# Performance work log

Measured on AMD Instinct MI355X. Metric: run time of the kernel, lower is better.

Reference implementation:

```python
import jax, jax.numpy as jnp
import numpy as np

# Dimensions
B, S, F, PATCH, D, H, NL, DFF, HOR = 512, 336, 12, 6, 512, 8, 6, 2048, 24
NP = S // PATCH        # 56 temporal patches
DH = D // H            # head dim = 64
EPS = 1e-5


def layer_norm(x, g, b):
    m = jnp.mean(x, axis=-1, keepdims=True)
    v = jnp.mean(jnp.square(x - m), axis=-1, keepdims=True)
    return (x - m) * jax.lax.rsqrt(v + EPS) * g + b


def alibi_bias(n_heads, n):
    # slopes = 2^(-8h/H), h = 1..H (standard ALiBi, H power of 2)
    slopes = 2.0 ** (-8.0 * jnp.arange(1, n_heads + 1, dtype=jnp.float32) / n_heads)
    pos = jnp.arange(n, dtype=jnp.float32)
    dist = jnp.abs(pos[:, None] - pos[None, :])         # [n, n]
    return -slopes[:, None, None] * dist                # [H, n, n]


def setup_inputs() -> dict:
    key = jax.random.key(0)
    ks = jax.random.split(key, 16)
    g = lambda k, shape: jax.random.normal(k, shape, dtype=jnp.float32) * 0.02
    return {
        "x": jax.random.normal(ks[0], (B, S, F), dtype=jnp.float32),
        "patch_W": g(ks[1], (PATCH * F, D)),
        "patch_b": jnp.zeros((D,), jnp.float32),
        "pos": g(ks[2], (NP, D)),
        "ln1_g": jnp.ones((NL, D), jnp.float32),
        "ln1_b": jnp.zeros((NL, D), jnp.float32),
        "Wq": g(ks[3], (NL, D, D)), "bq": jnp.zeros((NL, D), jnp.float32),
        "Wk": g(ks[4], (NL, D, D)), "bk": jnp.zeros((NL, D), jnp.float32),
        "Wv": g(ks[5], (NL, D, D)), "bv": jnp.zeros((NL, D), jnp.float32),
        "Wo": g(ks[6], (NL, D, D)), "bo": jnp.zeros((NL, D), jnp.float32),
        "ln2_g": jnp.ones((NL, D), jnp.float32),
        "ln2_b": jnp.zeros((NL, D), jnp.float32),
        "W1": g(ks[7], (NL, D, DFF)), "b1": jnp.zeros((NL, DFF), jnp.float32),
        "W2": g(ks[8], (NL, DFF, D)), "b2": jnp.zeros((NL, D), jnp.float32),
        "fn_g": jnp.ones((D,), jnp.float32),
        "fn_b": jnp.zeros((D,), jnp.float32),
        "head_W": g(ks[9], (D, HOR)),
        "head_b": jnp.zeros((HOR,), jnp.float32),
    }


def reference(x, patch_W, patch_b, pos, ln1_g, ln1_b, Wq, bq, Wk, bk, Wv, bv,
              Wo, bo, ln2_g, ln2_b, W1, b1, W2, b2, fn_g, fn_b, head_W, head_b):
    # Temporal patch embedding: (B,S,F) -> (B,NP,PATCH*F) -> Linear -> +pos
    h = x.reshape(B, NP, PATCH * F) @ patch_W + patch_b + pos  # [B, NP, D]
    bias = alibi_bias(H, NP)                                   # [H, NP, NP]
    scale = 1.0 / np.sqrt(DH).astype(np.float32)
    for l in range(NL):
        # Pre-LN multi-head attention with ALiBi temporal decay bias
        hn = layer_norm(h, ln1_g[l], ln1_b[l])
        q = (hn @ Wq[l] + bq[l]).reshape(B, NP, H, DH)
        k = (hn @ Wk[l] + bk[l]).reshape(B, NP, H, DH)
        v = (hn @ Wv[l] + bv[l]).reshape(B, NP, H, DH)
        sc = jnp.einsum('bqhd,bkhd->bhqk', q, k) * scale + bias[None]
        a = jax.nn.softmax(sc, axis=-1)
        o = jnp.einsum('bhqk,bkhd->bqhd', a, v).reshape(B, NP, D)
        h = h + (o @ Wo[l] + bo[l])
        # Pre-LN feedforward
        hn2 = layer_norm(h, ln2_g[l], ln2_b[l])
        h = h + (jax.nn.gelu(hn2 @ W1[l] + b1[l]) @ W2[l] + b2[l])
    pooled = jnp.mean(h, axis=1)                               # [B, D]
    out = layer_norm(pooled, fn_g, fn_b) @ head_W + head_b     # [B, HOR]
    return out
```

## Files before the change

### kernel.cpp

```cpp
#include <hip/hip_runtime.h>
#include <hip/hip_bf16.h>
#include <math.h>

#define D_      512
#define NPATCH  56
#define DFF_    2048
#define NLAYER  6
#define HEADS   8
#define DH_     64
#define HOR_    24
#define BATCH_  512
#define NTOK_   (BATCH_ * NPATCH)
#define KPAD    96

typedef __hip_bfloat16 bf16;
typedef __bf16 bf16x8 __attribute__((ext_vector_type(8)));
typedef float  f32x4  __attribute__((ext_vector_type(4)));

__device__ __forceinline__ void gload_lds16(const void* g, void* lds) {
    __builtin_amdgcn_global_load_lds(
        (const __attribute__((address_space(1))) unsigned int*)g,
        (__attribute__((address_space(3))) unsigned int*)lds, 16, 0, 0);
}

__device__ __forceinline__ float block_sum256(float v) {
    __shared__ float sm[4];
    const int lane = threadIdx.x & 63;
    const int w    = threadIdx.x >> 6;
    #pragma unroll
    for (int o = 32; o > 0; o >>= 1) v += __shfl_down(v, o);
    __syncthreads();
    if (lane == 0) sm[w] = v;
    __syncthreads();
    return sm[0] + sm[1] + sm[2] + sm[3];
}

__device__ __forceinline__ float gelu_fast(float xg) {
    const float e = __expf(1.5957691216057308f * (xg + 0.044715f * xg * xg * xg));
    return xg - xg * __builtin_amdgcn_rcpf(1.f + e);
}

__global__ __launch_bounds__(256) void transpose_bf16_k(
    const float* __restrict__ in, bf16* __restrict__ out, int R, int C,
    size_t in_ls, size_t out_ls)
{
    __shared__ float t[32][33];
    in  += (size_t)blockIdx.z * in_ls;
    out += (size_t)blockIdx.z * out_ls;
    const int c0 = blockIdx.x * 32, r0 = blockIdx.y * 32;
    const int x = threadIdx.x & 31, y = threadIdx.x >> 5;
    #pragma unroll
    for (int i = 0; i < 4; i++)
        t[y + i * 8][x] = in[(size_t)(r0 + y + i * 8) * C + c0 + x];
    __syncthreads();
    #pragma unroll
    for (int i = 0; i < 4; i++)
        out[(size_t)(c0 + y + i * 8) * R + r0 + x] = __float2bfloat16(t[x][y + i * 8]);
}

__global__ __launch_bounds__(256) void pwt_k(
    const float* __restrict__ W, bf16* __restrict__ out)
{
    const int idx = blockIdx.x * 256 + threadIdx.x;
    if (idx >= D_ * KPAD) return;
    const int n = idx / KPAD, kk = idx % KPAD;
    out[idx] = (kk < 72) ? __float2bfloat16(W[kk * D_ + n]) : __float2bfloat16(0.f);
}

__global__ __launch_bounds__(256) void xpad_k(
    const float* __restrict__ x, bf16* __restrict__ out)
{
    const size_t idx = (size_t)blockIdx.x * 256 + threadIdx.x;
    if (idx >= (size_t)NTOK_ * KPAD) return;
    const size_t row = idx / KPAD;
    const int kk = (int)(idx - row * KPAD);
    out[idx] = (kk < 72) ? __float2bfloat16(x[row * 72 + kk]) : __float2bfloat16(0.f);
}

__global__ __launch_bounds__(256) void bqkv_k(
    const float* __restrict__ bq, const float* __restrict__ bk,
    const float* __restrict__ bv, float* __restrict__ o)
{
    const int idx = blockIdx.x * 256 + threadIdx.x;
    if (idx >= NLAYER * 3 * D_) return;
    const int l = idx / (3 * D_), n = idx % (3 * D_);
    float v;
    if      (n < D_)     v = bq[l * D_ + n];
    else if (n < 2 * D_) v = bk[l * D_ + n - D_];
    else                 v = bv[l * D_ + n - 2 * D_];
    o[idx] = v;
}

__global__ __launch_bounds__(256) void layernorm_bf16_k(
    const bf16* __restrict__ x, const float* __restrict__ g,
    const float* __restrict__ b, bf16* __restrict__ y)
{
    const int w = threadIdx.x >> 6, lane = threadIdx.x & 63;
    const size_t row = (size_t)blockIdx.x * 4 + w;
    const bf16x8 a8 = *(const bf16x8*)((const __bf16*)x + row * D_ + lane * 8);
    float a[8];
    #pragma unroll
    for (int i = 0; i < 8; i++) a[i] = (float)a8[i];
    float s = 0.f;
    #pragma unroll
    for (int i = 0; i < 8; i++) s += a[i];
    #pragma unroll
    for (int o = 32; o > 0; o >>= 1) s += __shfl_xor(s, o);
    const float mean = s * (1.f / 512.f);
    float d[8];
    #pragma unroll
    for (int i = 0; i < 8; i++) d[i] = a[i] - mean;
    float v = 0.f;
    #pragma unroll
    for (int i = 0; i < 8; i++) v += d[i] * d[i];
    #pragma unroll
    for (int o = 32; o > 0; o >>= 1) v += __shfl_xor(v, o);
    const float rstd = rsqrtf(v * (1.f / 512.f) + 1e-5f);
    const float4 g0 = *(const float4*)(g + lane * 8);
    const float4 g1 = *(const float4*)(g + lane * 8 + 4);
    const float4 b0 = *(const float4*)(b + lane * 8);
    const float4 b1 = *(const float4*)(b + lane * 8 + 4);
    const float gg[8] = {g0.x, g0.y, g0.z, g0.w, g1.x, g1.y, g1.z, g1.w};
    const float bb[8] = {b0.x, b0.y, b0.z, b0.w, b1.x, b1.y, b1.z, b1.w};
    bf16x8 o8;
    #pragma unroll
    for (int i = 0; i < 8; i++) o8[i] = (__bf16)(d[i] * rstd * gg[i] + bb[i]);
    *(bf16x8*)((__bf16*)y + row * D_ + lane * 8) = o8;
}

template<bool GELU, bool RESID, bool POS, bool QKVSPLIT>
__global__ __launch_bounds__(512, 4) void gemm_bf16_k(
    const bf16* __restrict__ A, const bf16* __restrict__ Bt,
    const float* __restrict__ bias, const bf16* __restrict__ resid,
    const float* __restrict__ pos, bf16* __restrict__ Cp,
    bf16* __restrict__ vt, int M, int N, int K, int nx)
{
    __shared__ __align__(16) bf16 ABs[3][384 * 32];
    const int tid  = threadIdx.x;
    const int wid  = tid >> 6;
    const int lane = tid & 63;

    const int nwg = gridDim.x;
    const int q8 = nwg >> 3, r8 = nwg & 7;
    const int xcd = blockIdx.x & 7, idx8 = blockIdx.x >> 3;
    const int swz = (xcd < r8 ? xcd * (q8 + 1) : r8 * (q8 + 1) + (xcd - r8) * q8) + idx8;
    const int n0 = (swz % nx) * 256;
    const int m0 = (swz / nx) * 128;
    const int wr = wid >> 2, wc = wid & 3;

    f32x4 acc[4][4];
    #pragma unroll
    for (int m = 0; m < 4; m++)
        #pragma unroll
        for (int n = 0; n < 4; n++) acc[m][n] = f32x4{0.f, 0.f, 0.f, 0.f};

    const int srow = lane >> 2;
    const int schunk = ((lane & 3) ^ ((lane >> 3) & 3)) * 8;
    const bf16* sp[3];
    int soff[3];
    #pragma unroll
    for (int i = 0; i < 3; i++) {
        const int s = wid * 3 + i;
        soff[i] = s * 512;
        sp[i] = (s < 8)
            ? A  + (size_t)(m0 + s * 16 + srow) * K + schunk
            : Bt + (size_t)(n0 + (s - 8) * 16 + srow) * K + schunk;
    }

    const int fr = lane & 15;
    const int qg = lane >> 4;
    const int roff = fr * 32 + ((qg ^ ((fr >> 1) & 3)) * 8);

    const int nt = K >> 5;
    #define STAGE(buf, kt)  do {                                   \
        gload_lds16(sp[0] + ((kt) << 5), &ABs[buf][soff[0]]);      \
        gload_lds16(sp[1] + ((kt) << 5), &ABs[buf][soff[1]]);      \
        gload_lds16(sp[2] + ((kt) << 5), &ABs[buf][soff[2]]); } while (0)

    STAGE(0, 0);
    STAGE(1, 1);

    int cur = 0, nxt = 2;
    for (int t = 0; t < nt; t++) {
        if (t < nt - 1) asm volatile("s_waitcnt vmcnt(3)" ::: "memory");
        else            asm volatile("s_waitcnt vmcnt(0)" ::: "memory");
        __builtin_amdgcn_s_barrier();
        __builtin_amdgcn_sched_barrier(0);
        bf16x8 af[4], bg[4];
        #pragma unroll
        for (int m = 0; m < 4; m++)
            af[m] = *(const bf16x8*)&ABs[cur][(wr * 4 + m) * 512 + roff];
        #pragma unroll
        for (int n = 0; n < 4; n++)
            bg[n] = *(const bf16x8*)&ABs[cur][(8 + wc * 4 + n) * 512 + roff];
        if (t + 2 < nt) STAGE(nxt, t + 2);
        #pragma unroll
        for (int m = 0; m < 4; m++)
            #pragma unroll
            for (int n = 0; n < 4; n++)
                acc[m][n] = __builtin_amdgcn_mfma_f32_16x16x32_bf16(af[m], bg[n], acc[m][n], 0, 0, 0);
        cur = (cur == 2) ? 0 : cur + 1;
        nxt = (nxt == 2) ? 0 : nxt + 1;
    }
    #undef STAGE

    const int rq = qg * 4;
    #pragma unroll
    for (int m = 0; m < 4; m++) {
        #pragma unroll
        for (int n = 0; n < 4; n++) {
            const int col = n0 + wc * 64 + n * 16 + fr;
            const float bcol = bias[col];
            #pragma unroll
            for (int j = 0; j < 4; j++) {
                const int row = m0 + wr * 64 + m * 16 + rq + j;
                float c = acc[m][n][j] + bcol;
                if (GELU)  c = gelu_fast(c);
                if (RESID) c += __bfloat162float(resid[(size_t)row * N + col]);
                if (POS)   c += pos[(size_t)(row % NPATCH) * D_ + col];
                if (QKVSPLIT) {
                    if (col < 1024) {
                        Cp[(size_t)row * 1024 + col] = __float2bfloat16(c);
                    } else {
                        const int c2 = col - 1024, hh = c2 >> 6, dd = c2 & 63;
                        const int bb = row / NPATCH, pp = row - bb * NPATCH;
                        vt[(((size_t)bb * 8 + hh) * 64 + dd) * 64 + pp] = __float2bfloat16(c);
                    }
                } else {
                    Cp[(size_t)row * N + col] = __float2bfloat16(c);
                }
            }
        }
    }
}

__global__ __launch_bounds__(256) void attn_mfma_k(
    const bf16* __restrict__ qk, const bf16* __restrict__ vt,
    bf16* __restrict__ ao)
{
    __shared__ __align__(16) bf16 St[4][64 * 72];
    const int tid  = threadIdx.x;
    const int w    = tid >> 6, lane = tid & 63;
    const int bh   = blockIdx.x * 4 + w;
    const int b    = bh >> 3, hh = bh & 7;
    const int fr   = lane & 15;
    const int qg   = lane >> 4;
    const int kc   = qg * 8;

    const bf16* Qb = qk + (size_t)b * NPATCH * 1024 + hh * 64;
    const bf16* Kb = Qb + 512;
    const bf16* Vb = vt + (size_t)bh * 4096;

    bf16x8 qf[4][2], kf[4][2];
    #pragma unroll
    for (int m = 0; m < 4; m++)
        #pragma unroll
        for (int ks = 0; ks < 2; ks++) {
            qf[m][ks] = *(const bf16x8*)&Qb[(size_t)(m * 16 + fr) * 1024 + ks * 32 + kc];
            kf[m][ks] = *(const bf16x8*)&Kb[(size_t)(m * 16 + fr) * 1024 + ks * 32 + kc];
        }

    f32x4 acc[4][4];
    #pragma unroll
    for (int m = 0; m < 4; m++)
        #pragma unroll
        for (int n = 0; n < 4; n++) acc[m][n] = f32x4{0.f, 0.f, 0.f, 0.f};
    #pragma unroll
    for (int ks = 0; ks < 2; ks++)
        #pragma unroll
        for (int m = 0; m < 4; m++)
            #pragma unroll
            for (int n = 0; n < 4; n++)
                acc[m][n] = __builtin_amdgcn_mfma_f32_16x16x32_bf16(qf[m][ks], kf[n][ks], acc[m][n], 0, 0, 0);

    bf16x8 vf[4][2];
    #pragma unroll
    for (int n = 0; n < 4; n++)
        #pragma unroll
        for (int ks = 0; ks < 2; ks++)
            vf[n][ks] = *(const bf16x8*)&Vb[(size_t)(n * 16 + fr) * 64 + ks * 32 + kc];

    const float slope = exp2f(-(float)(hh + 1));
    bf16* Sw = St[w];
    #pragma unroll
    for (int m = 0; m < 4; m++) {
        #pragma unroll
        for (int j = 0; j < 4; j++) {
            const int r = m * 16 + qg * 4 + j;
            float s[4];
            #pragma unroll
            for (int n = 0; n < 4; n++) {
                const int col = n * 16 + fr;
                float sv = acc[m][n][j] * 0.125f - slope * fabsf((float)(r - col));
                s[n] = (col >= NPATCH) ? -1e30f : sv;
            }
            float mx = fmaxf(fmaxf(s[0], s[1]), fmaxf(s[2], s[3]));
            mx = fmaxf(mx, __shfl_xor(mx, 1));
            mx = fmaxf(mx, __shfl_xor(mx, 2));
            mx = fmaxf(mx, __shfl_xor(mx, 4));
            mx = fmaxf(mx, __shfl_xor(mx, 8));
            float p[4], sum = 0.f;
            #pragma unroll
            for (int n = 0; n < 4; n++) { p[n] = __expf(s[n] - mx); sum += p[n]; }
            sum += __shfl_xor(sum, 1);
            sum += __shfl_xor(sum, 2);
            sum += __shfl_xor(sum, 4);
            sum += __shfl_xor(sum, 8);
            const float inv = 1.f / sum;
            #pragma unroll
            for (int n = 0; n < 4; n++)
                Sw[r * 72 + n * 16 + fr] = __float2bfloat16(p[n] * inv);
        }
    }

    #pragma unroll
    for (int m = 0; m < 4; m++)
        #pragma unroll
        for (int n = 0; n < 4; n++) acc[m][n] = f32x4{0.f, 0.f, 0.f, 0.f};
    #pragma unroll
    for (int m = 0; m < 4; m++)
        #pragma unroll
        for (int ks = 0; ks < 2; ks++) {
            const bf16x8 pf = *(const bf16x8*)&Sw[(m * 16 + fr) * 72 + ks * 32 + kc];
            #pragma unroll
            for (int n = 0; n < 4; n++)
                acc[m][n] = __builtin_amdgcn_mfma_f32_16x16x32_bf16(pf, vf[n][ks], acc[m][n], 0, 0, 0);
        }

    bf16* Ob = ao + (size_t)b * NPATCH * 512 + hh * 64;
    #pragma unroll
    for (int m = 0; m < 4; m++)
        #pragma unroll
        for (int j = 0; j < 4; j++) {
            const int r = m * 16 + qg * 4 + j;
            if (r < NPATCH)
                #pragma unroll
                for (int n = 0; n < 4; n++)
                    Ob[(size_t)r * 512 + n * 16 + fr] = __float2bfloat16(acc[m][n][j]);
        }
}

__global__ __launch_bounds__(256) void head_k(
    const bf16* __restrict__ h, const float* __restrict__ g,
    const float* __restrict__ bb, const float* __restrict__ hW,
    const float* __restrict__ hb, float* __restrict__ out)
{
    const int b = blockIdx.x;
    __shared__ float row[D_];
    const int tid = threadIdx.x;
    float v0 = 0.f, v1 = 0.f;
    #pragma unroll
    for (int p = 0; p < NPATCH; p++) {
        const bf16* hr = h + (size_t)b * NPATCH * D_ + (size_t)p * D_;
        v0 += __bfloat162float(hr[tid]);
        v1 += __bfloat162float(hr[tid + 256]);
    }
    v0 *= (1.f / (float)NPATCH);
    v1 *= (1.f / (float)NPATCH);
    const float mean = block_sum256(v0 + v1) * (1.f / 512.f);
    const float d0 = v0 - mean, d1 = v1 - mean;
    const float var = block_sum256(d0 * d0 + d1 * d1) * (1.f / 512.f);
    const float rstd = rsqrtf(var + 1e-5f);
    row[tid]       = d0 * rstd * g[tid]       + bb[tid];
    row[tid + 256] = d1 * rstd * g[tid + 256] + bb[tid + 256];
    __syncthreads();
    if (tid < HOR_) {
        float acc = hb[tid];
        for (int kk = 0; kk < D_; kk++) acc = fmaf(row[kk], hW[kk * HOR_ + tid], acc);
        out[(size_t)b * HOR_ + tid] = acc;
    }
}

extern "C" void kernel_launch(void* const* d_in, const int* in_sizes, int n_in,
                              void* d_out, int out_size, void* d_ws, size_t ws_size,
                              hipStream_t stream)
{
    const float* x       = (const float*)d_in[0];
    const float* patch_W = (const float*)d_in[1];
    const float* patch_b = (const float*)d_in[2];
    const float* pos     = (const float*)d_in[3];
    const float* ln1_g   = (const float*)d_in[4];
    const float* ln1_b   = (const float*)d_in[5];
    const float* Wq      = (const float*)d_in[6];
    const float* bq      = (const float*)d_in[7];
    const float* Wk      = (const float*)d_in[8];
    const float* bk      = (const float*)d_in[9];
    const float* Wv      = (const float*)d_in[10];
    const float* bv      = (const float*)d_in[11];
    const float* Wo      = (const float*)d_in[12];
    const float* bo      = (const float*)d_in[13];
    const float* ln2_g   = (const float*)d_in[14];
    const float* ln2_b   = (const float*)d_in[15];
    const float* W1      = (const float*)d_in[16];
    const float* b1      = (const float*)d_in[17];
    const float* W2      = (const float*)d_in[18];
    const float* b2      = (const float*)d_in[19];
    const float* fn_g    = (const float*)d_in[20];
    const float* fn_b    = (const float*)d_in[21];
    const float* head_W  = (const float*)d_in[22];
    const float* head_b  = (const float*)d_in[23];
    float* out = (float*)d_out;

    const size_t WELEM  = (size_t)D_ * D_;
    const size_t WFELEM = (size_t)D_ * DFF_;
    bf16* wqkvt = (bf16*)d_ws;
    bf16* wot   = wqkvt + (size_t)NLAYER * 3 * WELEM;
    bf16* w1t   = wot   + (size_t)NLAYER * WELEM;
    bf16* w2t   = w1t   + (size_t)NLAYER * WFELEM;
    bf16* pwt   = w2t   + (size_t)NLAYER * WFELEM;
    float* bqkv = (float*)(pwt + (size_t)D_ * KPAD);
    bf16* xpad  = (bf16*)(bqkv + NLAYER * 3 * D_);
    char* wend  = (char*)(xpad + (size_t)NTOK_ * KPAD);
    const size_t FIXED = (size_t)(wend - (char*)d_ws);

    int BC = 16;
    for (int cand = BATCH_; cand >= 16; cand >>= 1) {
        const size_t need = FIXED + (size_t)cand * (56 * 5120 + 65536);
        if (need <= ws_size) { BC = cand; break; }
    }
    const int nChunks = BATCH_ / BC;
    const int CT = BC * NPATCH;
    const size_t TD = (size_t)CT * D_;

    bf16* h    = (bf16*)wend;
    bf16* hn   = h + TD;
    bf16* qk   = hn + TD;
    bf16* ao   = qk + (size_t)CT * 1024;
    bf16* vt   = ao + TD;
    bf16* mid  = qk;

    transpose_bf16_k<<<dim3(16, 16, NLAYER), 256, 0, stream>>>(
        Wq, wqkvt,                 D_, D_, WELEM, 3 * WELEM);
    transpose_bf16_k<<<dim3(16, 16, NLAYER), 256, 0, stream>>>(
        Wk, wqkvt + WELEM,         D_, D_, WELEM, 3 * WELEM);
    transpose_bf16_k<<<dim3(16, 16, NLAYER), 256, 0, stream>>>(
        Wv, wqkvt + 2 * WELEM,     D_, D_, WELEM, 3 * WELEM);
    transpose_bf16_k<<<dim3(16, 16, NLAYER), 256, 0, stream>>>(
        Wo, wot,                   D_, D_, WELEM, WELEM);
    transpose_bf16_k<<<dim3(64, 16, NLAYER), 256, 0, stream>>>(
        W1, w1t,                   D_, DFF_, WFELEM, WFELEM);
    transpose_bf16_k<<<dim3(16, 64, NLAYER), 256, 0, stream>>>(
        W2, w2t,                   DFF_, D_, WFELEM, WFELEM);
    pwt_k<<<(D_ * KPAD + 255) / 256, 256, 0, stream>>>(patch_W, pwt);
    bqkv_k<<<(NLAYER * 3 * D_ + 255) / 256, 256, 0, stream>>>(bq, bk, bv, bqkv);
    xpad_k<<<((size_t)NTOK_ * KPAD + 255) / 256, 256, 0, stream>>>(x, xpad);

    const int mt  = CT / 128;
    const int g1n = (D_ / 256) * mt;
    const int gqn = (3 * D_ / 256) * mt;
    const int g2n = (DFF_ / 256) * mt;

    for (int c = 0; c < nChunks; c++) {
        const size_t tok0 = (size_t)c * CT;

        gemm_bf16_k<false, false, true, false><<<g1n, 512, 0, stream>>>(
            xpad + tok0 * KPAD, pwt, patch_b, nullptr, pos, h, nullptr,
            CT, D_, KPAD, D_ / 256);

        for (int l = 0; l < NLAYER; l++) {
            layernorm_bf16_k<<<CT / 4, 256, 0, stream>>>(h, ln1_g + l * D_, ln1_b + l * D_, hn);
            gemm_bf16_k<false, false, false, true><<<gqn, 512, 0, stream>>>(
                hn, wqkvt + (size_t)l * 3 * WELEM, bqkv + l * 3 * D_, nullptr, nullptr,
                qk, vt, CT, 3 * D_, D_, 3 * D_ / 256);
            attn_mfma_k<<<BC * 2, 256, 0, stream>>>(qk, vt, ao);
            gemm_bf16_k<false, true, false, false><<<g1n, 512, 0, stream>>>(
                ao, wot + (size_t)l * WELEM, bo + l * D_, h, nullptr, h, nullptr,
                CT, D_, D_, D_ / 256);
            layernorm_bf16_k<<<CT / 4, 256, 0, stream>>>(h, ln2_g + l * D_, ln2_b + l * D_, hn);
            gemm_bf16_k<true, false, false, false><<<g2n, 512, 0, stream>>>(
                hn, w1t + (size_t)l * WFELEM, b1 + l * DFF_, nullptr, nullptr,
                mid, nullptr, CT, DFF_, D_, DFF_ / 256);
            gemm_bf16_k<false, true, false, false><<<g1n, 512, 0, stream>>>(
                mid, w2t + (size_t)l * WFELEM, b2 + l * D_, h, nullptr, h, nullptr,
                CT, D_, DFF_, D_ / 256);
        }

        head_k<<<BC, 256, 0, stream>>>(h, fn_g, fn_b, head_W, head_b,
                                       out + (size_t)c * BC * HOR_);
    }
}
```

Measured before the change: 1.977 ms.

## Fuse layernorm apply into GEMM A-operand load via precomputed row stats

Replaces the standalone layernorm kernel, which wrote a normalized bf16 copy of h, with a small row-statistics kernel that writes only mean and rstd per row. The QKV and FFN1 GEMMs then normalize their A fragments in registers, applying gamma and beta after the LDS read and before the MFMA. This removes a full activation write and re-read per layernorm and frees the hn buffer, which may allow a larger batch chunk. In exchange, every GEMM block normalizes A fragments each k-step, so the same rows are normalized repeatedly across N-tiles. The variance also switches to a one-pass E[x^2]-mean^2 formula, which carries some cancellation risk.

```diff
diff --git a/kernel.cpp b/kernel.cpp
--- a/kernel.cpp
+++ b/kernel.cpp
@@ -91,49 +91,31 @@
     o[idx] = v;
 }
 
-__global__ __launch_bounds__(256) void layernorm_bf16_k(
-    const bf16* __restrict__ x, const float* __restrict__ g,
-    const float* __restrict__ b, bf16* __restrict__ y)
+__global__ __launch_bounds__(256) void rowstats_k(
+    const bf16* __restrict__ x, float2* __restrict__ st)
 {
     const int w = threadIdx.x >> 6, lane = threadIdx.x & 63;
     const size_t row = (size_t)blockIdx.x * 4 + w;
     const bf16x8 a8 = *(const bf16x8*)((const __bf16*)x + row * D_ + lane * 8);
-    float a[8];
-    #pragma unroll
-    for (int i = 0; i < 8; i++) a[i] = (float)a8[i];
-    float s = 0.f;
-    #pragma unroll
-    for (int i = 0; i < 8; i++) s += a[i];
-    #pragma unroll
-    for (int o = 32; o > 0; o >>= 1) s += __shfl_xor(s, o);
-    const float mean = s * (1.f / 512.f);
-    float d[8];
-    #pragma unroll
-    for (int i = 0; i < 8; i++) d[i] = a[i] - mean;
-    float v = 0.f;
-    #pragma unroll
-    for (int i = 0; i < 8; i++) v += d[i] * d[i];
-    #pragma unroll
-    for (int o = 32; o > 0; o >>= 1) v += __shfl_xor(v, o);
-    const float rstd = rsqrtf(v * (1.f / 512.f) + 1e-5f);
-    const float4 g0 = *(const float4*)(g + lane * 8);
-    const float4 g1 = *(const float4*)(g + lane * 8 + 4);
-    const float4 b0 = *(const float4*)(b + lane * 8);
-    const float4 b1 = *(const float4*)(b + lane * 8 + 4);
-    const float gg[8] = {g0.x, g0.y, g0.z, g0.w, g1.x, g1.y, g1.z, g1.w};
-    const float bb[8] = {b0.x, b0.y, b0.z, b0.w, b1.x, b1.y, b1.z, b1.w};
-    bf16x8 o8;
-    #pragma unroll
-    for (int i = 0; i < 8; i++) o8[i] = (__bf16)(d[i] * rstd * gg[i] + bb[i]);
-    *(bf16x8*)((__bf16*)y + row * D_ + lane * 8) = o8;
-}
-
-template<bool GELU, bool RESID, bool POS, bool QKVSPLIT>
+    float s = 0.f, q = 0.f;
+    #pragma unroll
+    for (int i = 0; i < 8; i++) { const float a = (float)a8[i]; s += a; q += a * a; }
+    #pragma unroll
+    for (int o = 32; o > 0; o >>= 1) { s += __shfl_xor(s, o); q += __shfl_xor(q, o); }
+    if (lane == 0) {
+        const float mean = s * (1.f / 512.f);
+        const float var  = q * (1.f / 512.f) - mean * mean;
+        st[row] = make_float2(mean, rsqrtf(var + 1e-5f));
+    }
+}
+
+template<bool GELU, bool RESID, bool POS, bool QKVSPLIT, bool LNA>
 __global__ __launch_bounds__(512, 4) void gemm_bf16_k(
     const bf16* __restrict__ A, const bf16* __restrict__ Bt,
     const float* __restrict__ bias, const bf16* __restrict__ resid,
-    const float* __restrict__ pos, bf16* __restrict__ Cp,
-    bf16* __restrict__ vt, int M, int N, int K, int nx)
+    const float* __restrict__ pos, const float2* __restrict__ rowstat,
+    const float* __restrict__ lng, const float* __restrict__ lnb,
+    bf16* __restrict__ Cp, bf16* __restrict__ vt, int M, int N, int K, int nx)
 {
     __shared__ __align__(16) bf16 ABs[3][384 * 32];
     const int tid  = threadIdx.x;
@@ -171,6 +153,13 @@
     const int qg = lane >> 4;
     const int roff = fr * 32 + ((qg ^ ((fr >> 1) & 3)) * 8);
 
+    float2 rs[4];
+    if (LNA) {
+        #pragma unroll
+        for (int m = 0; m < 4; m++)
+            rs[m] = rowstat[m0 + wr * 64 + m * 16 + fr];
+    }
+
     const int nt = K >> 5;
     #define STAGE(buf, kt)  do {                                   \
         gload_lds16(sp[0] + ((kt) << 5), &ABs[buf][soff[0]]);      \
@@ -194,6 +183,20 @@
         for (int n = 0; n < 4; n++)
             bg[n] = *(const bf16x8*)&ABs[cur][(8 + wc * 4 + n) * 512 + roff];
         if (t + 2 < nt) STAGE(nxt, t + 2);
+        if (LNA) {
+            const int kbase = (t << 5) + (qg << 3);
+            const float4 g0 = *(const float4*)(lng + kbase);
+            const float4 g1 = *(const float4*)(lng + kbase + 4);
+            const float4 b0 = *(const float4*)(lnb + kbase);
+            const float4 b1 = *(const float4*)(lnb + kbase + 4);
+            const float gk[8] = {g0.x, g0.y, g0.z, g0.w, g1.x, g1.y, g1.z, g1.w};
+            const float bk[8] = {b0.x, b0.y, b0.z, b0.w, b1.x, b1.y, b1.z, b1.w};
+            #pragma unroll
+            for (int m = 0; m < 4; m++)
+                #pragma unroll
+                for (int e = 0; e < 8; e++)
+                    af[m][e] = (__bf16)((((float)af[m][e]) - rs[m].x) * rs[m].y * gk[e] + bk[e]);
+        }
         #pragma unroll
         for (int m = 0; m < 4; m++)
             #pragma unroll
@@ -415,7 +418,7 @@
 
     int BC = 16;
     for (int cand = BATCH_; cand >= 16; cand >>= 1) {
-        const size_t need = FIXED + (size_t)cand * (56 * 5120 + 65536);
+        const size_t need = FIXED + (size_t)cand * (56 * 4096 + 65536 + 56 * 8);
         if (need <= ws_size) { BC = cand; break; }
     }
     const int nChunks = BATCH_ / BC;
@@ -423,10 +426,10 @@
     const size_t TD = (size_t)CT * D_;
 
     bf16* h    = (bf16*)wend;
-    bf16* hn   = h + TD;
-    bf16* qk   = hn + TD;
+    bf16* qk   = h + TD;
     bf16* ao   = qk + (size_t)CT * 1024;
     bf16* vt   = ao + TD;
+    float2* stat = (float2*)(vt + (size_t)BC * 32768);
     bf16* mid  = qk;
 
     transpose_bf16_k<<<dim3(16, 16, NLAYER), 256, 0, stream>>>(
@@ -453,26 +456,28 @@
     for (int c = 0; c < nChunks; c++) {
         const size_t tok0 = (size_t)c * CT;
 
-        gemm_bf16_k<false, false, true, false><<<g1n, 512, 0, stream>>>(
-            xpad + tok0 * KPAD, pwt, patch_b, nullptr, pos, h, nullptr,
-            CT, D_, KPAD, D_ / 256);
+        gemm_bf16_k<false, false, true, false, false><<<g1n, 512, 0, stream>>>(
+            xpad + tok0 * KPAD, pwt, patch_b, nullptr, pos, nullptr, nullptr, nullptr,
+            h, nullptr, CT, D_, KPAD, D_ / 256);
 
         for (int l = 0; l < NLAYER; l++) {
-            layernorm_bf16_k<<<CT / 4, 256, 0, stream>>>(h, ln1_g + l * D_, ln1_b + l * D_, hn);
-            gemm_bf16_k<false, false, false, true><<<gqn, 512, 0, stream>>>(
-                hn, wqkvt + (size_t)l * 3 * WELEM, bqkv + l * 3 * D_, nullptr, nullptr,
+            rowstats_k<<<CT / 4, 256, 0, stream>>>(h, stat);
+            gemm_bf16_k<false, false, false, true, true><<<gqn, 512, 0, stream>>>(
+                h, wqkvt + (size_t)l * 3 * WELEM, bqkv + l * 3 * D_, nullptr, nullptr,
+                stat, ln1_g + l * D_, ln1_b + l * D_,
                 qk, vt, CT, 3 * D_, D_, 3 * D_ / 256);
             attn_mfma_k<<<BC * 2, 256, 0, stream>>>(qk, vt, ao);
-            gemm_bf16_k<false, true, false, false><<<g1n, 512, 0, stream>>>(
-                ao, wot + (size_t)l * WELEM, bo + l * D_, h, nullptr, h, nullptr,
-                CT, D_, D_, D_ / 256);
-            layernorm_bf16_k<<<CT / 4, 256, 0, stream>>>(h, ln2_g + l * D_, ln2_b + l * D_, hn);
-            gemm_bf16_k<true, false, false, false><<<g2n, 512, 0, stream>>>(
-                hn, w1t + (size_t)l * WFELEM, b1 + l * DFF_, nullptr, nullptr,
+            gemm_bf16_k<false, true, false, false, false><<<g1n, 512, 0, stream>>>(
+                ao, wot + (size_t)l * WELEM, bo + l * D_, h, nullptr, nullptr, nullptr, nullptr,
+                h, nullptr, CT, D_, D_, D_ / 256);
+            rowstats_k<<<CT / 4, 256, 0, stream>>>(h, stat);
+            gemm_bf16_k<true, false, false, false, true><<<g2n, 512, 0, stream>>>(
+                h, w1t + (size_t)l * WFELEM, b1 + l * DFF_, nullptr, nullptr,
+                stat, ln2_g + l * D_, ln2_b + l * D_,
                 mid, nullptr, CT, DFF_, D_, DFF_ / 256);
-            gemm_bf16_k<false, true, false, false><<<g1n, 512, 0, stream>>>(
-                mid, w2t + (size_t)l * WFELEM, b2 + l * D_, h, nullptr, h, nullptr,
-                CT, D_, DFF_, D_ / 256);
+            gemm_bf16_k<false, true, false, false, false><<<g1n, 512, 0, stream>>>(
+                mid, w2t + (size_t)l * WFELEM, b2 + l * D_, h, nullptr, nullptr, nullptr, nullptr,
+                h, nullptr, CT, D_, DFF_, D_ / 256);
         }
 
         head_k<<<BC, 256, 0, stream>>>(h, fn_g, fn_b, head_W, head_b,
```

Result: slower. 3.849 ms (+94.7%).
